# Optimization experiments

Measured on AMD Instinct MI355X. Metric: run time of the kernel, lower is better.

The kernel has to match this reference:

```python
import jax, jax.numpy as jnp
import numpy as np

# dims: batch, seq_len(N)=hidden(H) (required: layer>0 feeds H back into Linears sized N),
# features C, AATE dim A, layers L, decoder widths
B, N, C, A, H, L, FC, FFC = 256, 512, 64, 64, 512, 3, 256, 32


def setup_inputs() -> dict:
    key = jax.random.key(0)
    ks = jax.random.split(key, 24)
    def p(k, shape):
        return jax.random.normal(k, shape, jnp.float32) * 0.02
    return dict(
        x=jax.random.normal(ks[0], (B, N, C), jnp.float32),
        occ=jax.random.normal(ks[1], (B, N, 1), jnp.float32),
        proj_w=p(ks[2], (A, N)), proj_b=p(ks[3], (A,)),
        ll1_w=p(ks[4], (L, A, N)), ll1_b=p(ks[5], (L, A)),
        ll2_w=p(ks[6], (L, A, N)), ll2_b=p(ks[7], (L, A)),
        g1_w=p(ks[8], (L, 1, N + A)), g1_b=p(ks[9], (L, 1)),
        g2_w=p(ks[10], (L, 1, N + A)), g2_b=p(ks[11], (L, 1)),
        gc_w=p(ks[12], (L, H, 3 * N)), gc_b=p(ks[13], (L, H)),
        ta_w=p(ks[14], (H, H)), ta_b=p(ks[15], (H,)),
        d1_w=p(ks[16], (FC, H)), d1_b=p(ks[17], (FC,)),
        d2_w=p(ks[18], (1, FC)), d2_b=p(ks[19], (1,)),
        c1_w=p(ks[20], (FFC, C)), c1_b=p(ks[21], (FFC,)),
        c2_w=p(ks[22], (1, FFC)), c2_b=p(ks[23], (1,)),
    )


def _nconv(x, a):
    # x: [B,F,n,m], a: [B,m,n,v] -> [B,F,v,m]   (torch.einsum('bfnm,bmnv->bfvm'))
    return jnp.einsum('bfnm,bmnv->bfvm', x, a)


def reference(x, occ, proj_w, proj_b, ll1_w, ll1_b, ll2_w, ll2_b,
              g1_w, g1_b, g2_w, g2_b, gc_w, gc_b, ta_w, ta_b,
              d1_w, d1_b, d2_w, d2_b, c1_w, c1_b, c2_w, c2_b):
    Bn, Nn, Cn = x.shape
    An = proj_w.shape[0]
    xm = jnp.transpose(x, (0, 2, 1))[:, :, None, :]               # [B,C,1,N]  (M=1)
    proj = jnp.transpose(occ, (0, 2, 1)) @ proj_w.T + proj_b      # [B,1,A]
    # torch: repeat(M,1,C,1).view(B,M,C,A) -> tile along C; view(B,M,A,C) reinterleaves
    AATE = jnp.tile(proj[:, :, None, :], (1, 1, Cn, 1))           # [B,1,C,A]
    AATE_T = AATE.reshape(Bn, 1, An, Cn)                          # [B,1,A,C] (raw reshape, as in torch .view)
    for l in range(L):
        a_pc = jnp.transpose(AATE, (0, 2, 1, 3))                  # [B,C,1,A]
        at_pc = jnp.transpose(AATE_T, (0, 3, 1, 2))               # [B,C,1,A]
        m1 = jax.nn.relu(jnp.tanh(jnp.concatenate([xm, a_pc], -1) @ g1_w[l].T + g1_b[l]))   # [B,C,1,1]
        m2 = jax.nn.relu(jnp.tanh(jnp.concatenate([xm, at_pc], -1) @ g2_w[l].T + g2_b[l]))  # [B,C,1,1]
        e1 = jax.nn.softmax(jax.nn.relu(m1 * (xm @ ll1_w[l].T + ll1_b[l])), axis=-1)        # [B,C,1,A]
        e2 = jax.nn.softmax(jax.nn.relu(m2 * (xm @ ll2_w[l].T + ll2_b[l])), axis=-1)        # [B,C,1,A]
        e1 = AATE + jnp.transpose(e1, (0, 2, 1, 3))               # [B,1,C,A]
        e2 = AATE_T + jnp.transpose(e2, (0, 2, 3, 1))             # [B,1,A,C]
        adp = jax.nn.softmax(jax.nn.relu(e1 @ e2), axis=-1)       # [B,1,C,C] adaptive adjacency
        xg = jnp.transpose(xm, (0, 3, 1, 2))                      # [B,N,C,1]
        x1 = _nconv(xg, adp)
        x2 = _nconv(x1, adp)
        h = jnp.concatenate([xg, x1, x2], axis=1)                 # [B,3N,C,1]
        hh = jnp.einsum('bfcm,of->bocm', h, gc_w[l]) + gc_b[l][None, :, None, None]  # [B,H,C,1]
        xnew = jnp.transpose(jax.nn.relu(hh), (0, 2, 3, 1))       # [B,C,1,H]
        xm = (xm + xnew) if l > 0 else xnew                       # residual for layer>0
    z = xm.mean(axis=2)                                           # [B,C,H]  (mean over M=1)
    z = z @ ta_w.T + ta_b                                         # temporal_agg (Linear)
    d = jax.nn.relu(z @ d1_w.T + d1_b) @ d2_w.T + d2_b            # decoder -> [B,C,1]
    dp = jnp.transpose(d, (0, 2, 1))                              # [B,1,C]
    cd = jax.nn.relu(dp @ c1_w.T + c1_b) @ c2_w.T + c2_b          # channel_decoder -> [B,1,1]
    return jnp.abs(jnp.transpose(cd, (0, 2, 1)).squeeze(-1))      # [B,1] rul_prediction
```

## Files before the change

kernel.cpp:

```cpp
#include <hip/hip_runtime.h>

typedef unsigned short u16;
typedef __attribute__((ext_vector_type(8))) short short8;
typedef __attribute__((ext_vector_type(4))) float f32x4;


__device__ __forceinline__ u16 f2b(float f) {
    union { float f; unsigned int i; } v; v.f = f;
    unsigned int x = v.i;
    x += 0x7fffu + ((x >> 16) & 1u);
    return (u16)(x >> 16);
}
__device__ __forceinline__ float b2f(u16 u) {
    union { unsigned int i; float f; } v;
    v.i = ((unsigned int)u) << 16;
    return v.f;
}
__device__ __forceinline__ void gl_lds16(const u16* g, u16* l) {
    __builtin_amdgcn_global_load_lds((__attribute__((address_space(1))) void*)(u16*)g,
                                     (__attribute__((address_space(3))) void*)l, 16, 0, 0);
}

__global__ __launch_bounds__(256) void k_cvt(const float* __restrict__ src, u16* __restrict__ dst, int n4) {
    int i = blockIdx.x * 256 + threadIdx.x;
    if (i < n4) {
        float4 v = ((const float4*)src)[i];
        ushort4 o; o.x = f2b(v.x); o.y = f2b(v.y); o.z = f2b(v.z); o.w = f2b(v.w);
        ((ushort4*)dst)[i] = o;
    }
}

__global__ __launch_bounds__(256) void k_transpose(const float* __restrict__ x, u16* __restrict__ xmb) {
    __shared__ float tile[64][65];
    const int b  = blockIdx.y;
    const int n0 = blockIdx.x * 64;
    const int t  = threadIdx.x;
    const int c  = t & 63;
    const int dn = t >> 6;
#pragma unroll
    for (int i = 0; i < 16; ++i) {
        int nl = dn + i * 4;
        tile[c][nl] = x[((size_t)b * 512 + n0 + nl) * 64 + c];
    }
    __syncthreads();
    const int nl = t & 63;
    const int cb = (t >> 6) * 16;
#pragma unroll
    for (int i = 0; i < 16; ++i) {
        int c2 = cb + i;
        xmb[((size_t)b * 64 + c2) * 512 + n0 + nl] = f2b(tile[c2][nl]);
    }
}

__global__ __launch_bounds__(64) void k_proj(const float* __restrict__ occ, const float* __restrict__ pw,
                                             const float* __restrict__ pb, float* __restrict__ proj) {
    const int b = blockIdx.x;
    const int a = threadIdx.x;
    const float* ob = occ + (size_t)b * 512;
    const float* wr = pw + (size_t)a * 512;
    float acc = 0.f;
    for (int n = 0; n < 512; ++n) acc += ob[n] * wr[n];
    proj[b * 64 + a] = acc + pb[a];
}

__global__ __launch_bounds__(64) void k_pm(const u16* __restrict__ xmb,
                                           const float* __restrict__ g1w, const float* __restrict__ g1b,
                                           const float* __restrict__ g2w, const float* __restrict__ g2b,
                                           const float* __restrict__ proj, float* __restrict__ vb) {
    const int r = blockIdx.x;
    const int b = r >> 6, c = r & 63;
    const int lane = threadIdx.x;
    const u16* row = xmb + (size_t)r * 512 + lane * 8;
    uint4 xv = *(const uint4*)row;
    const u16* xp = (const u16*)&xv;
    float4 w1a = *(const float4*)(g1w + lane * 8);
    float4 w1b = *(const float4*)(g1w + lane * 8 + 4);
    float4 w2a = *(const float4*)(g2w + lane * 8);
    float4 w2b = *(const float4*)(g2w + lane * 8 + 4);
    float g1v[8] = {w1a.x, w1a.y, w1a.z, w1a.w, w1b.x, w1b.y, w1b.z, w1b.w};
    float g2v[8] = {w2a.x, w2a.y, w2a.z, w2a.w, w2b.x, w2b.y, w2b.z, w2b.w};
    float a1 = 0.f, a2 = 0.f;
#pragma unroll
    for (int e = 0; e < 8; ++e) {
        float xvf = b2f(xp[e]);
        a1 += xvf * g1v[e];
        a2 += xvf * g2v[e];
    }
    a1 += proj[b * 64 + lane] * g1w[512 + lane];
    a2 += proj[b * 64 + c]    * g2w[512 + lane];
    for (int off = 32; off; off >>= 1) { a1 += __shfl_xor(a1, off); a2 += __shfl_xor(a2, off); }
    float m1 = tanhf(a1 + g1b[0]); m1 = m1 > 0.f ? m1 : 0.f;
    float m2 = tanhf(a2 + g2b[0]); m2 = m2 > 0.f ? m2 : 0.f;
    const int a = lane;
    float s1 = m1 * vb[(size_t)r * 128 + a];       s1 = s1 > 0.f ? s1 : 0.f;
    float s2 = m2 * vb[(size_t)r * 128 + 64 + a];  s2 = s2 > 0.f ? s2 : 0.f;
    float mx1 = s1, mx2 = s2;
    for (int off = 32; off; off >>= 1) { mx1 = fmaxf(mx1, __shfl_xor(mx1, off)); mx2 = fmaxf(mx2, __shfl_xor(mx2, off)); }
    float e1 = expf(s1 - mx1), e2 = expf(s2 - mx2);
    float su1 = e1, su2 = e2;
    for (int off = 32; off; off >>= 1) { su1 += __shfl_xor(su1, off); su2 += __shfl_xor(su2, off); }
    vb[(size_t)r * 128 + a]      = proj[b * 64 + a] + e1 / su1;
    vb[(size_t)r * 128 + 64 + a] = proj[b * 64 + c] + e2 / su2;
}

__global__ __launch_bounds__(256) void k_adp(const float* __restrict__ vb, u16* __restrict__ adpT) {
    __shared__ float P1s[64][64];
    __shared__ float P2s[64][65];
    __shared__ __align__(16) u16 Tl[64 * 72];
    const int b = blockIdx.x;
    const int t = threadIdx.x;
#pragma unroll
    for (int i = 0; i < 16; ++i) {
        int idx = t + 256 * i;
        int c = idx >> 6, a = idx & 63;
        P1s[c][a] = vb[((size_t)b * 64 + c) * 128 + a];
        P2s[c][a] = vb[((size_t)b * 64 + c) * 128 + 64 + a];
    }
    __syncthreads();
    const int lane = t & 63;
    const int w = t >> 6;
    for (int ci = 0; ci < 16; ++ci) {
        int c = w + ci * 4;
        float s = 0.f;
        for (int a = 0; a < 64; ++a) s += P1s[c][a] * P2s[lane][a];
        s = fmaxf(s, 0.f);
        float mx = s;
        for (int off = 32; off; off >>= 1) mx = fmaxf(mx, __shfl_xor(mx, off));
        float e = expf(s - mx);
        float su = e;
        for (int off = 32; off; off >>= 1) su += __shfl_xor(su, off);
        Tl[lane * 72 + c] = f2b(e / su);
    }
    __syncthreads();
    const int v = t >> 2, ck = (t & 3) * 16;
    u16* dst = adpT + ((size_t)b * 64 + v) * 64 + ck;
    *(uint4*)dst       = *(const uint4*)&Tl[v * 72 + ck];
    *(uint4*)(dst + 8) = *(const uint4*)&Tl[v * 72 + ck + 8];
}

__global__ __launch_bounds__(256) void k_nconv2(const u16* __restrict__ Xbf, const u16* __restrict__ adpT,
                                                u16* __restrict__ x1bf, u16* __restrict__ x2bf) {
    __shared__ __align__(16) u16 Ts[64 * 72];
    __shared__ __align__(16) u16 Xs[128 * 72];
    const int b  = blockIdx.y;
    const int n0 = blockIdx.x * 128;
    const int t  = threadIdx.x;
    const int lane = t & 63, w = t >> 6;
    const int lrow = lane & 15, q = lane >> 4;
    const int wn = w * 32;

    {
        int v = t >> 2, ck = (t & 3) * 8;
        const u16* src = adpT + ((size_t)b * 64 + v) * 64;
        *(uint4*)&Ts[v * 72 + ck]      = *(const uint4*)(src + ck);
        *(uint4*)&Ts[v * 72 + ck + 32] = *(const uint4*)(src + ck + 32);
    }
    {
        int c = t >> 2;
        const u16* xr = Xbf + ((size_t)b * 64 + c) * 512 + n0;
#pragma unroll
        for (int j = 0; j < 4; ++j) {
            int nn = j * 32 + (t & 3) * 8;
            uint4 vv = *(const uint4*)(xr + nn);
            const u16* pv = (const u16*)&vv;
#pragma unroll
            for (int e = 0; e < 8; ++e) Xs[(nn + e) * 72 + c] = pv[e];
        }
    }
    __syncthreads();

    const f32x4 zero = {0.f, 0.f, 0.f, 0.f};
    f32x4 acc[4][2];
#pragma unroll
    for (int mt = 0; mt < 4; ++mt)
#pragma unroll
        for (int nt = 0; nt < 2; ++nt) acc[mt][nt] = zero;

#pragma unroll
    for (int ks = 0; ks < 2; ++ks) {
        short8 af[4], bfr[2];
#pragma unroll
        for (int mt = 0; mt < 4; ++mt) af[mt]  = *(const short8*)&Ts[(mt * 16 + lrow) * 72 + ks * 32 + q * 8];
#pragma unroll
        for (int nt = 0; nt < 2; ++nt) bfr[nt] = *(const short8*)&Xs[(wn + nt * 16 + lrow) * 72 + ks * 32 + q * 8];
#pragma unroll
        for (int mt = 0; mt < 4; ++mt)
#pragma unroll
            for (int nt = 0; nt < 2; ++nt)
                acc[mt][nt] = __builtin_amdgcn_mfma_f32_16x16x32_bf16(af[mt], bfr[nt], acc[mt][nt], 0, 0, 0);
    }
    __syncthreads();

#pragma unroll
    for (int mt = 0; mt < 4; ++mt)
#pragma unroll
        for (int nt = 0; nt < 2; ++nt) {
            int nl = wn + nt * 16 + lrow;
            ushort4 u;
            u.x = f2b(acc[mt][nt][0]); u.y = f2b(acc[mt][nt][1]);
            u.z = f2b(acc[mt][nt][2]); u.w = f2b(acc[mt][nt][3]);
            *(ushort4*)&Xs[nl * 72 + mt * 16 + q * 4] = u;
#pragma unroll
            for (int i = 0; i < 4; ++i)
                x1bf[((size_t)(b * 64 + mt * 16 + q * 4 + i)) * 512 + n0 + nl] = ((const u16*)&u)[i];
        }
    __syncthreads();

    f32x4 acc2[4][2];
#pragma unroll
    for (int mt = 0; mt < 4; ++mt)
#pragma unroll
        for (int nt = 0; nt < 2; ++nt) acc2[mt][nt] = zero;
#pragma unroll
    for (int ks = 0; ks < 2; ++ks) {
        short8 af[4], bfr[2];
#pragma unroll
        for (int mt = 0; mt < 4; ++mt) af[mt]  = *(const short8*)&Ts[(mt * 16 + lrow) * 72 + ks * 32 + q * 8];
#pragma unroll
        for (int nt = 0; nt < 2; ++nt) bfr[nt] = *(const short8*)&Xs[(wn + nt * 16 + lrow) * 72 + ks * 32 + q * 8];
#pragma unroll
        for (int mt = 0; mt < 4; ++mt)
#pragma unroll
            for (int nt = 0; nt < 2; ++nt)
                acc2[mt][nt] = __builtin_amdgcn_mfma_f32_16x16x32_bf16(af[mt], bfr[nt], acc2[mt][nt], 0, 0, 0);
    }
#pragma unroll
    for (int mt = 0; mt < 4; ++mt)
#pragma unroll
        for (int nt = 0; nt < 2; ++nt) {
            int nl = wn + nt * 16 + lrow;
#pragma unroll
            for (int i = 0; i < 4; ++i)
                x2bf[((size_t)(b * 64 + mt * 16 + q * 4 + i)) * 512 + n0 + nl] = f2b(acc2[mt][nt][i]);
        }
}

template<int BM, int BN>
__global__ __launch_bounds__(256) void mfma_gemm(
    const u16* __restrict__ A0, const u16* __restrict__ A1, const u16* __restrict__ A2,
    const u16* __restrict__ W0, const u16* __restrict__ W1, int nsplit,
    const float* __restrict__ bias0, const float* __restrict__ bias1,
    const u16* __restrict__ resbf, float* __restrict__ out, u16* __restrict__ outbf,
    int N, int K, int relu)
{
    constexpr int MT = BM / 32;
    constexpr int NT = BN / 32;
    constexpr int AI = BM / 16;
    constexpr int BI = BN / 16;
    constexpr int CH = (BM + BN) * 32;
    __shared__ __align__(16) u16 SM[4 * CH];
    const int t    = threadIdx.x;
    const int m0   = blockIdx.x * BM;
    const int n0   = blockIdx.y * BN;
    const int lane = t & 63;
    const int w    = t >> 6;
    const int wm   = (w >> 1) * (BM / 2);
    const int wn   = (w & 1) * (BN / 2);
    const int lrow = lane & 15;
    const int q    = lane >> 4;
    const int sr16 = lane >> 2;
    const int sp   = lane & 3;

    auto stage32 = [&](int k0, int buf, int ch) {
        u16* As = SM + (buf * 2 + ch) * CH;
        u16* Bs = As + BM * 32;
        const u16* Abase = A0;
        int kloc = k0;
        if (K > 512) {
            int seg = k0 >> 9;
            Abase = (seg == 0) ? A0 : ((seg == 1) ? A1 : A2);
            kloc = k0 & 511;
        }
#pragma unroll
        for (int jj = 0; jj < AI / 4; ++jj) {
            int j = jj * 4 + w;
            int row = j * 16 + sr16;
            int c = (sp - (row >> 1)) & 3;
            gl_lds16(Abase + (size_t)(m0 + row) * 512 + kloc + c * 8, As + j * 512);
        }
#pragma unroll
        for (int jj = 0; jj < BI / 4; ++jj) {
            int j = jj * 4 + w;
            int row = j * 16 + sr16;
            int n = n0 + row;
            const u16* wr = (n < nsplit) ? (W0 + (size_t)n * K) : (W1 + (size_t)(n - nsplit) * K);
            int c = (sp - (row >> 1)) & 3;
            gl_lds16(wr + k0 + c * 8, Bs + j * 512);
        }
    };

    const f32x4 zero = {0.f, 0.f, 0.f, 0.f};
    f32x4 acc[MT][NT];
#pragma unroll
    for (int i = 0; i < MT; ++i)
#pragma unroll
        for (int j = 0; j < NT; ++j) acc[i][j] = zero;

    stage32(0, 0, 0);
    stage32(32, 0, 1);
    const int iters = K >> 6;
    int buf = 0;
    for (int it = 0; it < iters; ++it) {
        __syncthreads();
        if (it + 1 < iters) {
            stage32((it + 1) * 64, buf ^ 1, 0);
            stage32((it + 1) * 64 + 32, buf ^ 1, 1);
        }
#pragma unroll
        for (int ch = 0; ch < 2; ++ch) {
            const u16* As = SM + (buf * 2 + ch) * CH;
            const u16* Bs = As + BM * 32;
            short8 af[MT], bfr[NT];
#pragma unroll
            for (int mt = 0; mt < MT; ++mt) {
                int row = wm + mt * 16 + lrow;
                int p = (q + (row >> 1)) & 3;
                af[mt] = *(const short8*)&As[row * 32 + p * 8];
            }
#pragma unroll
            for (int nt = 0; nt < NT; ++nt) {
                int row = wn + nt * 16 + lrow;
                int p = (q + (row >> 1)) & 3;
                bfr[nt] = *(const short8*)&Bs[row * 32 + p * 8];
            }
#pragma unroll
            for (int mt = 0; mt < MT; ++mt)
#pragma unroll
                for (int nt = 0; nt < NT; ++nt)
                    acc[mt][nt] = __builtin_amdgcn_mfma_f32_16x16x32_bf16(af[mt], bfr[nt], acc[mt][nt], 0, 0, 0);
        }
        buf ^= 1;
    }

#pragma unroll
    for (int mt = 0; mt < MT; ++mt) {
        int mb = m0 + wm + mt * 16 + q * 4;
#pragma unroll
        for (int nt = 0; nt < NT; ++nt) {
            int n = n0 + wn + nt * 16 + lrow;
            float bvv = (n < nsplit) ? bias0[n] : bias1[n - nsplit];
#pragma unroll
            for (int i = 0; i < 4; ++i) {
                float v = acc[mt][nt][i] + bvv;
                if (relu) v = fmaxf(v, 0.f);
                if (resbf) v += b2f(resbf[(size_t)(mb + i) * N + n]);
                if (out) out[(size_t)(mb + i) * N + n] = v;
                if (outbf) outbf[(size_t)(mb + i) * N + n] = f2b(v);
            }
        }
    }
}

__global__ __launch_bounds__(256) void k_dvec(const float* __restrict__ tmat, const float* __restrict__ d2w,
                                              const float* __restrict__ d2b, float* __restrict__ dvec) {
    const int r = blockIdx.x * 4 + (threadIdx.x >> 6);
    const int lane = threadIdx.x & 63;
    const float* row = tmat + (size_t)r * 256;
    float acc = 0.f;
    for (int f = lane; f < 256; f += 64) acc += row[f] * d2w[f];
    for (int off = 32; off; off >>= 1) acc += __shfl_xor(acc, off);
    if (lane == 0) dvec[r] = acc + d2b[0];
}

__global__ __launch_bounds__(64) void k_final(const float* __restrict__ dvec, const float* __restrict__ c1w,
                                              const float* __restrict__ c1b, const float* __restrict__ c2w,
                                              const float* __restrict__ c2b, float* __restrict__ out) {
    const int b = blockIdx.x;
    const int f = threadIdx.x;
    float part = 0.f;
    if (f < 32) {
        float acc = c1b[f];
        const float* dr = dvec + b * 64;
        for (int c = 0; c < 64; ++c) acc += dr[c] * c1w[f * 64 + c];
        acc = acc > 0.f ? acc : 0.f;
        part = acc * c2w[f];
    }
    for (int off = 32; off; off >>= 1) part += __shfl_xor(part, off);
    if (f == 0) out[b] = fabsf(part + c2b[0]);
}

extern "C" void kernel_launch(void* const* d_in, const int* in_sizes, int n_in,
                              void* d_out, int out_size, void* d_ws, size_t ws_size,
                              hipStream_t stream) {
    const float* x     = (const float*)d_in[0];
    const float* occ   = (const float*)d_in[1];
    const float* projw = (const float*)d_in[2];
    const float* projb = (const float*)d_in[3];
    const float* ll1w  = (const float*)d_in[4];
    const float* ll1b  = (const float*)d_in[5];
    const float* ll2w  = (const float*)d_in[6];
    const float* ll2b  = (const float*)d_in[7];
    const float* g1w   = (const float*)d_in[8];
    const float* g1b   = (const float*)d_in[9];
    const float* g2w   = (const float*)d_in[10];
    const float* g2b   = (const float*)d_in[11];
    const float* gcw   = (const float*)d_in[12];
    const float* gcb   = (const float*)d_in[13];
    const float* taw   = (const float*)d_in[14];
    const float* tab   = (const float*)d_in[15];
    const float* d1w   = (const float*)d_in[16];
    const float* d1b   = (const float*)d_in[17];
    const float* d2w   = (const float*)d_in[18];
    const float* d2b   = (const float*)d_in[19];
    const float* c1w   = (const float*)d_in[20];
    const float* c1b   = (const float*)d_in[21];
    const float* c2w   = (const float*)d_in[22];
    const float* c2b   = (const float*)d_in[23];

    const size_t MR = (size_t)16384 * 512;
    float* ws   = (float*)d_ws;
    float* x2T  = ws;
    float* vbuf = x2T + (size_t)16384 * 256;
    float* proj = vbuf + (size_t)16384 * 128;
    float* dvec = proj + 16384;
    u16* bfb     = (u16*)(dvec + 16384);
    u16* xmA_bf  = bfb;
    u16* xmB_bf  = xmA_bf + MR;
    u16* x1_bf   = xmB_bf + MR;
    u16* x2_bf   = x1_bf + MR;
    u16* x1T_bf  = x2_bf + MR;
    u16* adpT_bf = x1T_bf + MR;
    u16* ll1w_bf = adpT_bf + (size_t)16384 * 64;
    u16* ll2w_bf = ll1w_bf + 98304;
    u16* gcw_bf  = ll2w_bf + 98304;
    u16* taw_bf  = gcw_bf + 2359296;
    u16* d1w_bf  = taw_bf + 262144;

    k_cvt<<<96,   256, 0, stream>>>(ll1w, ll1w_bf, 98304 / 4);
    k_cvt<<<96,   256, 0, stream>>>(ll2w, ll2w_bf, 98304 / 4);
    k_cvt<<<2304, 256, 0, stream>>>(gcw,  gcw_bf,  2359296 / 4);
    k_cvt<<<256,  256, 0, stream>>>(taw,  taw_bf,  262144 / 4);
    k_cvt<<<128,  256, 0, stream>>>(d1w,  d1w_bf,  131072 / 4);

    k_transpose<<<dim3(8, 256), 256, 0, stream>>>(x, xmA_bf);
    k_proj<<<256, 64, 0, stream>>>(occ, projw, projb, proj);

    u16* cur_bf = xmA_bf;
    u16* nxt_bf = xmB_bf;
    for (int l = 0; l < 3; ++l) {
        mfma_gemm<64, 64><<<dim3(256, 2), 256, 0, stream>>>(
            cur_bf, nullptr, nullptr,
            ll1w_bf + (size_t)l * 32768, ll2w_bf + (size_t)l * 32768, 64,
            ll1b + l * 64, ll2b + l * 64, nullptr, vbuf, nullptr, 128, 512, 0);
        k_pm<<<16384, 64, 0, stream>>>(cur_bf, g1w + l * 576, g1b + l, g2w + l * 576, g2b + l, proj, vbuf);
        k_adp<<<256, 256, 0, stream>>>(vbuf, adpT_bf);
        k_nconv2<<<dim3(4, 256), 256, 0, stream>>>(cur_bf, adpT_bf, x1_bf, x2_bf);
        mfma_gemm<128, 64><<<dim3(128, 8), 256, 0, stream>>>(
            cur_bf, x1_bf, x2_bf,
            gcw_bf + (size_t)l * 786432, gcw_bf + (size_t)l * 786432, 512,
            gcb + l * 512, gcb + l * 512, (l > 0 ? cur_bf : nullptr), nullptr, nxt_bf, 512, 1536, 1);
        { u16* tb = cur_bf; cur_bf = nxt_bf; nxt_bf = tb; }
    }
    mfma_gemm<128, 64><<<dim3(128, 8), 256, 0, stream>>>(
        cur_bf, nullptr, nullptr, taw_bf, taw_bf, 512, tab, tab, nullptr, nullptr, x1T_bf, 512, 512, 0);
    mfma_gemm<64, 64><<<dim3(256, 4), 256, 0, stream>>>(
        x1T_bf, nullptr, nullptr, d1w_bf, d1w_bf, 256, d1b, d1b, nullptr, x2T, nullptr, 256, 512, 1);
    k_dvec<<<4096, 256, 0, stream>>>(x2T, d2w, d2b, dvec);
    k_final<<<256, 64, 0, stream>>>(dvec, c1w, c1b, c2w, c2b, (float*)d_out);
}
```

Baseline: 488.3 us.

## Fuse weight conversions, gating with adjacency, decoder tail; shrink GEMM K-step

Five weight-conversion launches become one kernel that indexes into a contiguous bf16 weight buffer. The per-row gating/softmax kernel is merged into the adjacency kernel, so the gated vectors stay in shared memory and skip a global round trip. The two decoder-tail kernels are merged into one per-batch block. The MFMA GEMM now stages 32-wide K chunks double-buffered instead of 64-wide, halving shared memory but adding more barriers per K.

```diff
diff --git a/kernel.cpp b/kernel.cpp
--- a/kernel.cpp
+++ b/kernel.cpp
@@ -21,13 +21,21 @@
                                      (__attribute__((address_space(3))) void*)l, 16, 0, 0);
 }
 
-__global__ __launch_bounds__(256) void k_cvt(const float* __restrict__ src, u16* __restrict__ dst, int n4) {
+__global__ __launch_bounds__(256) void k_cvt_all(const float* __restrict__ ll1w, const float* __restrict__ ll2w,
+                                                 const float* __restrict__ gcw, const float* __restrict__ taw,
+                                                 const float* __restrict__ d1w, u16* __restrict__ dst) {
     int i = blockIdx.x * 256 + threadIdx.x;
-    if (i < n4) {
-        float4 v = ((const float4*)src)[i];
-        ushort4 o; o.x = f2b(v.x); o.y = f2b(v.y); o.z = f2b(v.z); o.w = f2b(v.w);
-        ((ushort4*)dst)[i] = o;
-    }
+    if (i >= 737280) return;
+    const float* src;
+    int off;
+    if (i < 24576)       { src = ll1w; off = i; }
+    else if (i < 49152)  { src = ll2w; off = i - 24576; }
+    else if (i < 638976) { src = gcw;  off = i - 49152; }
+    else if (i < 704512) { src = taw;  off = i - 638976; }
+    else                 { src = d1w;  off = i - 704512; }
+    float4 v = ((const float4*)src)[off];
+    ushort4 o; o.x = f2b(v.x); o.y = f2b(v.y); o.z = f2b(v.z); o.w = f2b(v.w);
+    ((ushort4*)dst)[i] = o;
 }
 
 __global__ __launch_bounds__(256) void k_transpose(const float* __restrict__ x, u16* __restrict__ xmb) {
@@ -63,62 +71,54 @@
     proj[b * 64 + a] = acc + pb[a];
 }
 
-__global__ __launch_bounds__(64) void k_pm(const u16* __restrict__ xmb,
-                                           const float* __restrict__ g1w, const float* __restrict__ g1b,
-                                           const float* __restrict__ g2w, const float* __restrict__ g2b,
-                                           const float* __restrict__ proj, float* __restrict__ vb) {
-    const int r = blockIdx.x;
-    const int b = r >> 6, c = r & 63;
-    const int lane = threadIdx.x;
-    const u16* row = xmb + (size_t)r * 512 + lane * 8;
-    uint4 xv = *(const uint4*)row;
-    const u16* xp = (const u16*)&xv;
-    float4 w1a = *(const float4*)(g1w + lane * 8);
-    float4 w1b = *(const float4*)(g1w + lane * 8 + 4);
-    float4 w2a = *(const float4*)(g2w + lane * 8);
-    float4 w2b = *(const float4*)(g2w + lane * 8 + 4);
-    float g1v[8] = {w1a.x, w1a.y, w1a.z, w1a.w, w1b.x, w1b.y, w1b.z, w1b.w};
-    float g2v[8] = {w2a.x, w2a.y, w2a.z, w2a.w, w2b.x, w2b.y, w2b.z, w2b.w};
-    float a1 = 0.f, a2 = 0.f;
-#pragma unroll
-    for (int e = 0; e < 8; ++e) {
-        float xvf = b2f(xp[e]);
-        a1 += xvf * g1v[e];
-        a2 += xvf * g2v[e];
-    }
-    a1 += proj[b * 64 + lane] * g1w[512 + lane];
-    a2 += proj[b * 64 + c]    * g2w[512 + lane];
-    for (int off = 32; off; off >>= 1) { a1 += __shfl_xor(a1, off); a2 += __shfl_xor(a2, off); }
-    float m1 = tanhf(a1 + g1b[0]); m1 = m1 > 0.f ? m1 : 0.f;
-    float m2 = tanhf(a2 + g2b[0]); m2 = m2 > 0.f ? m2 : 0.f;
-    const int a = lane;
-    float s1 = m1 * vb[(size_t)r * 128 + a];       s1 = s1 > 0.f ? s1 : 0.f;
-    float s2 = m2 * vb[(size_t)r * 128 + 64 + a];  s2 = s2 > 0.f ? s2 : 0.f;
-    float mx1 = s1, mx2 = s2;
-    for (int off = 32; off; off >>= 1) { mx1 = fmaxf(mx1, __shfl_xor(mx1, off)); mx2 = fmaxf(mx2, __shfl_xor(mx2, off)); }
-    float e1 = expf(s1 - mx1), e2 = expf(s2 - mx2);
-    float su1 = e1, su2 = e2;
-    for (int off = 32; off; off >>= 1) { su1 += __shfl_xor(su1, off); su2 += __shfl_xor(su2, off); }
-    vb[(size_t)r * 128 + a]      = proj[b * 64 + a] + e1 / su1;
-    vb[(size_t)r * 128 + 64 + a] = proj[b * 64 + c] + e2 / su2;
-}
-
-__global__ __launch_bounds__(256) void k_adp(const float* __restrict__ vb, u16* __restrict__ adpT) {
+__global__ __launch_bounds__(256) void k_pmadp(const u16* __restrict__ xmb, const float* __restrict__ vbuf,
+                                               const float* __restrict__ g1w, const float* __restrict__ g1b,
+                                               const float* __restrict__ g2w, const float* __restrict__ g2b,
+                                               const float* __restrict__ proj, u16* __restrict__ adpT) {
+    __shared__ float g1s[576], g2s[576], prj[64];
     __shared__ float P1s[64][64];
     __shared__ float P2s[64][65];
     __shared__ __align__(16) u16 Tl[64 * 72];
     const int b = blockIdx.x;
     const int t = threadIdx.x;
-#pragma unroll
-    for (int i = 0; i < 16; ++i) {
-        int idx = t + 256 * i;
-        int c = idx >> 6, a = idx & 63;
-        P1s[c][a] = vb[((size_t)b * 64 + c) * 128 + a];
-        P2s[c][a] = vb[((size_t)b * 64 + c) * 128 + 64 + a];
-    }
-    __syncthreads();
-    const int lane = t & 63;
-    const int w = t >> 6;
+    const int lane = t & 63, w = t >> 6;
+    if (t < 144) {
+        *(float4*)&g1s[t * 4] = *(const float4*)(g1w + t * 4);
+        *(float4*)&g2s[t * 4] = *(const float4*)(g2w + t * 4);
+    }
+    if (t >= 240) *(float4*)&prj[(t - 240) * 4] = *(const float4*)(proj + b * 64 + (t - 240) * 4);
+    __syncthreads();
+    float S1 = 0.f, G2 = 0.f;
+#pragma unroll
+    for (int a = 0; a < 64; ++a) { S1 += prj[a] * g1s[512 + a]; G2 += g2s[512 + a]; }
+    const float b1 = g1b[0], b2v = g2b[0];
+#pragma unroll 4
+    for (int ci = 0; ci < 16; ++ci) {
+        int c = w + ci * 4;
+        int r = b * 64 + c;
+        uint4 xv = *(const uint4*)(xmb + (size_t)r * 512 + lane * 8);
+        const u16* xp = (const u16*)&xv;
+        float a1 = 0.f, a2 = 0.f;
+#pragma unroll
+        for (int e = 0; e < 8; ++e) {
+            float xf = b2f(xp[e]);
+            a1 += xf * g1s[lane * 8 + e];
+            a2 += xf * g2s[lane * 8 + e];
+        }
+        for (int off = 32; off; off >>= 1) { a1 += __shfl_xor(a1, off); a2 += __shfl_xor(a2, off); }
+        float m1 = tanhf(a1 + S1 + b1);          m1 = m1 > 0.f ? m1 : 0.f;
+        float m2 = tanhf(a2 + prj[c] * G2 + b2v); m2 = m2 > 0.f ? m2 : 0.f;
+        float s1 = fmaxf(m1 * vbuf[(size_t)r * 128 + lane], 0.f);
+        float s2 = fmaxf(m2 * vbuf[(size_t)r * 128 + 64 + lane], 0.f);
+        float mx1 = s1, mx2 = s2;
+        for (int off = 32; off; off >>= 1) { mx1 = fmaxf(mx1, __shfl_xor(mx1, off)); mx2 = fmaxf(mx2, __shfl_xor(mx2, off)); }
+        float e1 = expf(s1 - mx1), e2 = expf(s2 - mx2);
+        float su1 = e1, su2 = e2;
+        for (int off = 32; off; off >>= 1) { su1 += __shfl_xor(su1, off); su2 += __shfl_xor(su2, off); }
+        P1s[c][lane] = prj[lane] + e1 / su1;
+        P2s[c][lane] = prj[c]    + e2 / su2;
+    }
+    __syncthreads();
     for (int ci = 0; ci < 16; ++ci) {
         int c = w + ci * 4;
         float s = 0.f;
@@ -247,8 +247,8 @@
     constexpr int NT = BN / 32;
     constexpr int AI = BM / 16;
     constexpr int BI = BN / 16;
-    constexpr int CH = (BM + BN) * 32;
-    __shared__ __align__(16) u16 SM[4 * CH];
+    constexpr int TILE = (BM + BN) * 32;
+    __shared__ __align__(16) u16 SM[2 * TILE];
     const int t    = threadIdx.x;
     const int m0   = blockIdx.x * BM;
     const int n0   = blockIdx.y * BN;
@@ -261,8 +261,8 @@
     const int sr16 = lane >> 2;
     const int sp   = lane & 3;
 
-    auto stage32 = [&](int k0, int buf, int ch) {
-        u16* As = SM + (buf * 2 + ch) * CH;
+    auto stage = [&](int k0, int buf) {
+        u16* As = SM + buf * TILE;
         u16* Bs = As + BM * 32;
         const u16* Abase = A0;
         int kloc = k0;
@@ -296,39 +296,32 @@
 #pragma unroll
         for (int j = 0; j < NT; ++j) acc[i][j] = zero;
 
-    stage32(0, 0, 0);
-    stage32(32, 0, 1);
-    const int iters = K >> 6;
+    stage(0, 0);
+    const int iters = K >> 5;
     int buf = 0;
     for (int it = 0; it < iters; ++it) {
         __syncthreads();
-        if (it + 1 < iters) {
-            stage32((it + 1) * 64, buf ^ 1, 0);
-            stage32((it + 1) * 64 + 32, buf ^ 1, 1);
-        }
-#pragma unroll
-        for (int ch = 0; ch < 2; ++ch) {
-            const u16* As = SM + (buf * 2 + ch) * CH;
-            const u16* Bs = As + BM * 32;
-            short8 af[MT], bfr[NT];
-#pragma unroll
-            for (int mt = 0; mt < MT; ++mt) {
-                int row = wm + mt * 16 + lrow;
-                int p = (q + (row >> 1)) & 3;
-                af[mt] = *(const short8*)&As[row * 32 + p * 8];
-            }
-#pragma unroll
-            for (int nt = 0; nt < NT; ++nt) {
-                int row = wn + nt * 16 + lrow;
-                int p = (q + (row >> 1)) & 3;
-                bfr[nt] = *(const short8*)&Bs[row * 32 + p * 8];
-            }
-#pragma unroll
-            for (int mt = 0; mt < MT; ++mt)
-#pragma unroll
-                for (int nt = 0; nt < NT; ++nt)
-                    acc[mt][nt] = __builtin_amdgcn_mfma_f32_16x16x32_bf16(af[mt], bfr[nt], acc[mt][nt], 0, 0, 0);
-        }
+        if (it + 1 < iters) stage((it + 1) * 32, buf ^ 1);
+        const u16* As = SM + buf * TILE;
+        const u16* Bs = As + BM * 32;
+        short8 af[MT], bfr[NT];
+#pragma unroll
+        for (int mt = 0; mt < MT; ++mt) {
+            int row = wm + mt * 16 + lrow;
+            int p = (q + (row >> 1)) & 3;
+            af[mt] = *(const short8*)&As[row * 32 + p * 8];
+        }
+#pragma unroll
+        for (int nt = 0; nt < NT; ++nt) {
+            int row = wn + nt * 16 + lrow;
+            int p = (q + (row >> 1)) & 3;
+            bfr[nt] = *(const short8*)&Bs[row * 32 + p * 8];
+        }
+#pragma unroll
+        for (int mt = 0; mt < MT; ++mt)
+#pragma unroll
+            for (int nt = 0; nt < NT; ++nt)
+                acc[mt][nt] = __builtin_amdgcn_mfma_f32_16x16x32_bf16(af[mt], bfr[nt], acc[mt][nt], 0, 0, 0);
         buf ^= 1;
     }
 
@@ -351,32 +344,36 @@
     }
 }
 
-__global__ __launch_bounds__(256) void k_dvec(const float* __restrict__ tmat, const float* __restrict__ d2w,
-                                              const float* __restrict__ d2b, float* __restrict__ dvec) {
-    const int r = blockIdx.x * 4 + (threadIdx.x >> 6);
-    const int lane = threadIdx.x & 63;
-    const float* row = tmat + (size_t)r * 256;
-    float acc = 0.f;
-    for (int f = lane; f < 256; f += 64) acc += row[f] * d2w[f];
-    for (int off = 32; off; off >>= 1) acc += __shfl_xor(acc, off);
-    if (lane == 0) dvec[r] = acc + d2b[0];
-}
-
-__global__ __launch_bounds__(64) void k_final(const float* __restrict__ dvec, const float* __restrict__ c1w,
-                                              const float* __restrict__ c1b, const float* __restrict__ c2w,
-                                              const float* __restrict__ c2b, float* __restrict__ out) {
-    const int b = blockIdx.x;
-    const int f = threadIdx.x;
-    float part = 0.f;
-    if (f < 32) {
-        float acc = c1b[f];
-        const float* dr = dvec + b * 64;
-        for (int c = 0; c < 64; ++c) acc += dr[c] * c1w[f * 64 + c];
-        acc = acc > 0.f ? acc : 0.f;
-        part = acc * c2w[f];
-    }
-    for (int off = 32; off; off >>= 1) part += __shfl_xor(part, off);
-    if (f == 0) out[b] = fabsf(part + c2b[0]);
+__global__ __launch_bounds__(256) void k_dec(const float* __restrict__ x2T, const float* __restrict__ d2w,
+                                             const float* __restrict__ d2b, const float* __restrict__ c1w,
+                                             const float* __restrict__ c1b, const float* __restrict__ c2w,
+                                             const float* __restrict__ c2b, float* __restrict__ out) {
+    __shared__ float dv[64];
+    __shared__ float d2s[256];
+    const int b = blockIdx.x, t = threadIdx.x;
+    const int lane = t & 63, w = t >> 6;
+    if (t < 64) *(float4*)&d2s[t * 4] = *(const float4*)(d2w + t * 4);
+    __syncthreads();
+#pragma unroll 4
+    for (int ci = 0; ci < 16; ++ci) {
+        int c = w + ci * 4;
+        const float* row = x2T + (size_t)(b * 64 + c) * 256;
+        float acc = row[lane] * d2s[lane] + row[64 + lane] * d2s[64 + lane]
+                  + row[128 + lane] * d2s[128 + lane] + row[192 + lane] * d2s[192 + lane];
+        for (int off = 32; off; off >>= 1) acc += __shfl_xor(acc, off);
+        if (lane == 0) dv[c] = acc + d2b[0];
+    }
+    __syncthreads();
+    if (w == 0) {
+        float part = 0.f;
+        if (lane < 32) {
+            float acc = c1b[lane];
+            for (int c = 0; c < 64; ++c) acc += dv[c] * c1w[lane * 64 + c];
+            part = fmaxf(acc, 0.f) * c2w[lane];
+        }
+        for (int off = 32; off; off >>= 1) part += __shfl_xor(part, off);
+        if (lane == 0) out[b] = fabsf(part + c2b[0]);
+    }
 }
 
 extern "C" void kernel_launch(void* const* d_in, const int* in_sizes, int n_in,
@@ -412,26 +409,21 @@
     float* x2T  = ws;
     float* vbuf = x2T + (size_t)16384 * 256;
     float* proj = vbuf + (size_t)16384 * 128;
-    float* dvec = proj + 16384;
-    u16* bfb     = (u16*)(dvec + 16384);
+    u16* bfb     = (u16*)(proj + 16384);
     u16* xmA_bf  = bfb;
     u16* xmB_bf  = xmA_bf + MR;
     u16* x1_bf   = xmB_bf + MR;
     u16* x2_bf   = x1_bf + MR;
     u16* x1T_bf  = x2_bf + MR;
     u16* adpT_bf = x1T_bf + MR;
-    u16* ll1w_bf = adpT_bf + (size_t)16384 * 64;
+    u16* wb      = adpT_bf + (size_t)16384 * 64;
+    u16* ll1w_bf = wb;
     u16* ll2w_bf = ll1w_bf + 98304;
     u16* gcw_bf  = ll2w_bf + 98304;
     u16* taw_bf  = gcw_bf + 2359296;
     u16* d1w_bf  = taw_bf + 262144;
 
-    k_cvt<<<96,   256, 0, stream>>>(ll1w, ll1w_bf, 98304 / 4);
-    k_cvt<<<96,   256, 0, stream>>>(ll2w, ll2w_bf, 98304 / 4);
-    k_cvt<<<2304, 256, 0, stream>>>(gcw,  gcw_bf,  2359296 / 4);
-    k_cvt<<<256,  256, 0, stream>>>(taw,  taw_bf,  262144 / 4);
-    k_cvt<<<128,  256, 0, stream>>>(d1w,  d1w_bf,  131072 / 4);
-
+    k_cvt_all<<<2880, 256, 0, stream>>>(ll1w, ll2w, gcw, taw, d1w, wb);
     k_transpose<<<dim3(8, 256), 256, 0, stream>>>(x, xmA_bf);
     k_proj<<<256, 64, 0, stream>>>(occ, projw, projb, proj);
 
@@ -442,8 +434,8 @@
             cur_bf, nullptr, nullptr,
             ll1w_bf + (size_t)l * 32768, ll2w_bf + (size_t)l * 32768, 64,
             ll1b + l * 64, ll2b + l * 64, nullptr, vbuf, nullptr, 128, 512, 0);
-        k_pm<<<16384, 64, 0, stream>>>(cur_bf, g1w + l * 576, g1b + l, g2w + l * 576, g2b + l, proj, vbuf);
-        k_adp<<<256, 256, 0, stream>>>(vbuf, adpT_bf);
+        k_pmadp<<<256, 256, 0, stream>>>(cur_bf, vbuf, g1w + l * 576, g1b + l,
+                                         g2w + l * 576, g2b + l, proj, adpT_bf);
         k_nconv2<<<dim3(4, 256), 256, 0, stream>>>(cur_bf, adpT_bf, x1_bf, x2_bf);
         mfma_gemm<128, 64><<<dim3(128, 8), 256, 0, stream>>>(
             cur_bf, x1_bf, x2_bf,
@@ -455,6 +447,5 @@
         cur_bf, nullptr, nullptr, taw_bf, taw_bf, 512, tab, tab, nullptr, nullptr, x1T_bf, 512, 512, 0);
     mfma_gemm<64, 64><<<dim3(256, 4), 256, 0, stream>>>(
         x1T_bf, nullptr, nullptr, d1w_bf, d1w_bf, 256, d1b, d1b, nullptr, x2T, nullptr, 256, 512, 1);
-    k_dvec<<<4096, 256, 0, stream>>>(x2T, d2w, d2b, dvec);
-    k_final<<<256, 64, 0, stream>>>(dvec, c1w, c1b, c2w, c2b, (float*)d_out);
-}
+    k_dec<<<256, 256, 0, stream>>>(x2T, d2w, d2b, c1w, c1b, c2w, c2b, (float*)d_out);
+}
```

Result: faster. 468.9 us (-4.0%).
